# Kernel optimization log

Measured on AMD Instinct MI355X. Metric: run time of the kernel, lower is better.

The kernel has to match this reference:

```python
import jax, jax.numpy as jnp
import numpy as np

B, C, H, W = 2, 64, 128, 128
KH = KW = 3
K = KH * KW
PAD = 1
GROUPS = 8          # conv groups
OFF_GROUPS = 8      # offset groups (offset channels = 2*OFF_GROUPS*K = 144)
NEG_SLOPE = 0.1


def setup_inputs() -> dict:
    key = jax.random.key(0)
    ks = jax.random.split(key, 8)
    s = lambda fan: 1.0 / np.sqrt(fan)
    return {
        "previous_features": jax.random.normal(ks[0], (B, C, H, W), jnp.float32),
        "offsets": jax.random.normal(ks[1], (B, 2 * OFF_GROUPS * K, H, W), jnp.float32),
        "dcn_weight": jax.random.normal(ks[2], (C, C // GROUPS, KH, KW), jnp.float32) * s((C // GROUPS) * K),
        "dcn_bias": jax.random.normal(ks[3], (C,), jnp.float32) * 0.01,
        "w1": jax.random.normal(ks[4], (C, 2 * C, KH, KW), jnp.float32) * s(2 * C * K),
        "b1": jax.random.normal(ks[5], (C,), jnp.float32) * 0.01,
        "w2": jax.random.normal(ks[6], (C, C, KH, KW), jnp.float32) * s(C * K),
        "b2": jax.random.normal(ks[7], (C,), jnp.float32) * 0.01,
    }


def _deform_conv2d(x, offsets, weight, bias):
    """torchvision DeformConv2d, stride=1, pad=1, dil=1, 3x3.
    x: [B,C,H,W]; offsets: [B, 2*og*K, H, W] with per-tap (dy, dx) pairs.
    """
    b, c, h, w = x.shape
    og = offsets.shape[1] // (2 * K)
    cg_off = c // og
    # [B, og, K, 2, H, W] -> dy, dx each [B, og, K, H, W]
    off = offsets.reshape(b, og, K, 2, h, w)
    dy, dx = off[:, :, :, 0], off[:, :, :, 1]
    # base sampling grid per kernel tap
    by = jnp.repeat(jnp.arange(KH), KW).astype(x.dtype)   # [K]
    bx = jnp.tile(jnp.arange(KW), KH).astype(x.dtype)     # [K]
    py = jnp.arange(h, dtype=x.dtype)[None, None, None, :, None] - PAD \
         + by[None, None, :, None, None] + dy              # [B,og,K,H,W]
    px = jnp.arange(w, dtype=x.dtype)[None, None, None, None, :] - PAD \
         + bx[None, None, :, None, None] + dx

    y0 = jnp.floor(py); x0 = jnp.floor(px)
    wy = py - y0;       wx = px - x0
    y0i = y0.astype(jnp.int32); x0i = x0.astype(jnp.int32)

    xg = x.reshape(b, og, cg_off, h * w)  # channel-grouped, flat spatial

    def samp(yi, xi):
        valid = (yi >= 0) & (yi < h) & (xi >= 0) & (xi < w)
        idx = jnp.clip(yi, 0, h - 1) * w + jnp.clip(xi, 0, w - 1)   # [B,og,K,H,W]
        v = jnp.take_along_axis(xg, idx.reshape(b, og, 1, K * h * w), axis=-1)
        v = v.reshape(b, og, cg_off, K, h, w)
        return v * valid[:, :, None].astype(x.dtype)

    v00 = samp(y0i,     x0i)
    v01 = samp(y0i,     x0i + 1)
    v10 = samp(y0i + 1, x0i)
    v11 = samp(y0i + 1, x0i + 1)
    wy_ = wy[:, :, None]; wx_ = wx[:, :, None]  # [B,og,1,K,H,W]
    sampled = (v00 * (1 - wy_) * (1 - wx_) + v01 * (1 - wy_) * wx_
               + v10 * wy_ * (1 - wx_) + v11 * wy_ * wx_)   # [B,og,Cg,K,H,W]

    g = c // weight.shape[1]
    cg = c // g
    cols = sampled.reshape(b, g, cg, K, h, w)                # channel order preserved
    w_g = weight.reshape(g, cg, cg, K)                       # [g, cout/g, cin/g, K]
    out = jnp.einsum('goik,bgikhw->bgohw', w_g, cols).reshape(b, c, h, w)
    return out + bias[None, :, None, None]


def _conv3x3(x, w, b):
    out = jax.lax.conv_general_dilated(
        x, w, window_strides=(1, 1), padding='SAME',
        dimension_numbers=('NCHW', 'OIHW', 'NCHW'))
    return out + b[None, :, None, None]


def _lrelu(x):
    return jnp.where(x >= 0, x, NEG_SLOPE * x)


def reference(previous_features, offsets, dcn_weight, dcn_bias, w1, b1, w2, b2):
    aligned = _deform_conv2d(previous_features, offsets, dcn_weight, dcn_bias)
    r = jnp.concatenate([aligned, previous_features], axis=1)
    r = _lrelu(_conv3x3(r, w1, b1))
    r = _lrelu(_conv3x3(r, w2, b2))
    return aligned + r
```

## Files before the change

kernel.cpp:

```cpp
#include <hip/hip_runtime.h>
#include <stdint.h>

typedef short short8 __attribute__((ext_vector_type(8)));
typedef float f32x4 __attribute__((ext_vector_type(4)));
typedef unsigned int u32x4 __attribute__((ext_vector_type(4)));
typedef unsigned int u32x2 __attribute__((ext_vector_type(2)));

constexpr int B_ = 2, C_ = 64, H_ = 128, W_ = 128, HW_ = H_ * W_;
constexpr float NEG_SLOPE = 0.1f;

__device__ inline unsigned short f2bf(float f) {
    union { float f; unsigned u; } c; c.f = f;
    unsigned r = c.u + 0x7FFFu + ((c.u >> 16) & 1u);
    return (unsigned short)(r >> 16);
}
__device__ inline float bf2f(unsigned short s) {
    union { unsigned u; float f; } c; c.u = ((unsigned)s) << 16; return c.f;
}
__device__ inline float bflo(unsigned u) {
    union { unsigned u; float f; } c; c.u = u << 16; return c.f;
}
__device__ inline float bfhi(unsigned u) {
    union { unsigned u; float f; } c; c.u = u & 0xFFFF0000u; return c.f;
}

__global__ __launch_bounds__(256) void prep_pack(
    const float* __restrict__ x,  const float* __restrict__ w1,
    const float* __restrict__ w2, const float* __restrict__ dw,
    unsigned short* __restrict__ x_g, unsigned short* __restrict__ w1a,
    unsigned short* __restrict__ w2a, unsigned short* __restrict__ dwr)
{
    __shared__ unsigned short t[64][72];
    const int bx = blockIdx.x;
    const int tid = threadIdx.x;

    if (bx < 512) {
        const int b  = bx >> 8;
        const int p0 = (bx & 255) * 64;
#pragma unroll
        for (int u = tid; u < 4096; u += 256) {
            const int c = u >> 6, pp = u & 63;
            t[pp][c ^ ((pp & 7) << 3)] = f2bf(x[((size_t)b * 64 + c) * HW_ + p0 + pp]);
        }
        __syncthreads();
#pragma unroll
        for (int u = tid; u < 512; u += 256) {
            const int g = u >> 6, pp = u & 63;
            const u32x4 v = *(const u32x4*)&t[pp][(g ^ (pp & 7)) * 8];
            *(u32x4*)(x_g + (((size_t)b * 8 + g) * HW_ + p0 + pp) * 8) = v;
        }
        return;
    }

    const int idx = (bx - 512) * 256 + tid;
    if (idx < 64 * 1152) {
        const int ici = idx & 31, t2 = idx >> 5;
        const int oc = t2 & 63, ks = t2 >> 6;
        const int icc = ks / 9, tap = ks - icc * 9;
        w1a[idx] = f2bf(w1[(oc * 128 + icc * 32 + ici) * 9 + tap]);
    }
    if (idx < 64 * 576) {
        const int ici = idx & 31, t2 = idx >> 5;
        const int oc = t2 & 63, ks = t2 >> 6;
        const int icc = ks / 9, tap = ks - icc * 9;
        w2a[idx] = f2bf(w2[(oc * 64 + icc * 32 + ici) * 9 + tap]);
    }
    if (idx < 8 * 3 * 64 * 8) {
        const int g = idx / 1536, r = idx - g * 1536;
        const int c = r / 512, r2 = r - c * 512;
        const int lane = r2 >> 3, j = r2 & 7;
        const int hi = lane >> 4, l15 = lane & 15;
        const int tp = c * 4 + hi;
        float v = 0.f;
        if (l15 < 8 && tp < 9) v = dw[((g * 8 + l15) * 8 + j) * 9 + tp];
        dwr[idx] = f2bf(v);
    }
}

__global__ __launch_bounds__(256) void dcn_mfma(
    const unsigned short* __restrict__ x_g,
    const float* __restrict__ off,
    const unsigned short* __restrict__ dwr,
    const float* __restrict__ bias,
    unsigned short* __restrict__ al_cl)
{
    const int tid  = threadIdx.x;
    const int wv   = tid >> 6;
    const int lane = tid & 63;
    const int hi   = lane >> 4;
    const int l15  = lane & 15;
    const int tile = blockIdx.x;
    const int b    = tile >> 10;
    const int p    = ((tile & 1023) << 4) + l15;
    const int h    = p >> 7;
    const int w    = p & (W_ - 1);

#pragma unroll
    for (int gi = 0; gi < 2; ++gi) {
        const int g = wv + gi * 4;
        const unsigned short* xg = x_g + ((size_t)b * 8 + g) * HW_ * 8;
        const float* offp = off + ((size_t)b * 144 + g * 18) * HW_ + p;

        float dy0 = offp[(hi * 2 + 0) * HW_];
        float dx0 = offp[(hi * 2 + 1) * HW_];
        float dy1 = offp[((4 + hi) * 2 + 0) * HW_];
        float dx1 = offp[((4 + hi) * 2 + 1) * HW_];
        float dy2 = 0.f, dx2 = 0.f;
        if (hi == 0) { dy2 = offp[16 * HW_]; dx2 = offp[17 * HW_]; }

        u32x4 cr[3][4];
        float fw[3][4];
#pragma unroll
        for (int s = 0; s < 3; ++s) {
            const bool active = (s < 2) || (hi == 0);
            if (active) {
                const int t = s * 4 + hi;
                const float dy = (s == 0) ? dy0 : (s == 1) ? dy1 : dy2;
                const float dx = (s == 0) ? dx0 : (s == 1) ? dx1 : dx2;
                const float py = (float)(h - 1 + t / 3) + dy;
                const float px = (float)(w - 1 + t % 3) + dx;
                const float y0f = floorf(py), x0f = floorf(px);
                const int y0 = (int)y0f, x0 = (int)x0f;
                const int y1 = y0 + 1,  x1 = x0 + 1;
                const float wy = py - y0f, wx = px - x0f;

                const bool vy0 = (unsigned)y0 < (unsigned)H_;
                const bool vy1 = (unsigned)y1 < (unsigned)H_;
                const bool vx0 = (unsigned)x0 < (unsigned)W_;
                const bool vx1 = (unsigned)x1 < (unsigned)W_;

                fw[s][0] = (vy0 && vx0) ? (1.f - wy) * (1.f - wx) : 0.f;
                fw[s][1] = (vy0 && vx1) ? (1.f - wy) * wx         : 0.f;
                fw[s][2] = (vy1 && vx0) ? wy * (1.f - wx)         : 0.f;
                fw[s][3] = (vy1 && vx1) ? wy * wx                 : 0.f;

                const int cy0 = min(max(y0, 0), H_ - 1);
                const int cy1 = min(max(y1, 0), H_ - 1);
                const int cx0 = min(max(x0, 0), W_ - 1);
                const int cx1 = min(max(x1, 0), W_ - 1);

                cr[s][0] = *(const u32x4*)(xg + (size_t)(cy0 * W_ + cx0) * 8);
                cr[s][1] = *(const u32x4*)(xg + (size_t)(cy0 * W_ + cx1) * 8);
                cr[s][2] = *(const u32x4*)(xg + (size_t)(cy1 * W_ + cx0) * 8);
                cr[s][3] = *(const u32x4*)(xg + (size_t)(cy1 * W_ + cx1) * 8);
            }
        }

        f32x4 acc = (f32x4){0.f, 0.f, 0.f, 0.f};
#pragma unroll
        for (int s = 0; s < 3; ++s) {
            short8 bfr = (short8){0, 0, 0, 0, 0, 0, 0, 0};
            if ((s < 2) || (hi == 0)) {
                unsigned rq[4];
#pragma unroll
                for (int q = 0; q < 4; ++q) {
                    const float lo = fw[s][0] * bflo(cr[s][0][q]) + fw[s][1] * bflo(cr[s][1][q])
                                   + fw[s][2] * bflo(cr[s][2][q]) + fw[s][3] * bflo(cr[s][3][q]);
                    const float hi_ = fw[s][0] * bfhi(cr[s][0][q]) + fw[s][1] * bfhi(cr[s][1][q])
                                    + fw[s][2] * bfhi(cr[s][2][q]) + fw[s][3] * bfhi(cr[s][3][q]);
                    asm("v_cvt_pk_bf16_f32 %0, %1, %2" : "=v"(rq[q]) : "v"(lo), "v"(hi_));
                }
                bfr = *(const short8*)rq;
            }
            const short8 afr = *(const short8*)(dwr + ((g * 3 + s) * 64 + lane) * 8);
            acc = __builtin_amdgcn_mfma_f32_16x16x32_bf16(afr, bfr, acc, 0, 0, 0);
        }

        if (hi < 2) {
            unsigned short o4[4];
#pragma unroll
            for (int r = 0; r < 4; ++r)
                o4[r] = f2bf(acc[r] + bias[g * 8 + hi * 4 + r]);
            *(u32x2*)(al_cl + ((size_t)b * HW_ + p) * 64 + g * 8 + hi * 4) = *(u32x2*)o4;
        }
    }
}

template <int CIN, bool FINAL>
__global__ __launch_bounds__(256) void conv_mfma(
    const unsigned short* __restrict__ in0,
    const unsigned short* __restrict__ x_g,
    const unsigned short* __restrict__ wa,
    const float* __restrict__ bias,
    const unsigned short* __restrict__ resid_cl,
    float* __restrict__ outf,
    unsigned short* __restrict__ outb)
{
    constexpr int NICC = CIN / 32;
    __shared__ unsigned short b_lds[2][3 * 66 * 32];

    const int tid  = threadIdx.x;
    const int lane = tid & 63;
    const int l15  = lane & 15;
    const int hi   = lane >> 4;
    const int wp   = (tid >> 6) & 1;
    const int wo   = tid >> 7;
    const int ct   = blockIdx.x;
    const int row  = blockIdx.y;
    const int b    = blockIdx.z;
    const int col0 = ct * 64;
    const int oc0w = wo * 32;

    f32x4 acc[2][2];
#pragma unroll
    for (int fm = 0; fm < 2; ++fm)
#pragma unroll
        for (int fn = 0; fn < 2; ++fn)
            acc[fm][fn] = (f32x4){0.f, 0.f, 0.f, 0.f};

    u32x4 sreg[4];

    auto ldregs = [&](int icc) {
#pragma unroll
        for (int t = 0; t < 4; ++t) {
            const int u = tid + t * 256;
            u32x4 v = (u32x4){0u, 0u, 0u, 0u};
            if (u < 792) {
                const int icq = u & 3, rc = u >> 2;
                const int ri = rc / 66, hc = rc - ri * 66;
                const int gr = row + ri - 1, gc = col0 + hc - 1;
                if ((unsigned)gr < 128u && (unsigned)gc < 128u) {
                    const int pix = gr * 128 + gc;
                    if (CIN == 64 || icc < 2)
                        v = *(const u32x4*)(in0 + ((size_t)b * HW_ + pix) * 64
                                             + icc * 32 + icq * 8);
                    else {
                        const int g = (icc - 2) * 4 + icq;
                        v = *(const u32x4*)(x_g + (((size_t)b * 8 + g) * HW_ + pix) * 8);
                    }
                }
            }
            sreg[t] = v;
        }
    };

    auto dswrite = [&](int buf) {
        char* bp = (char*)b_lds[buf];
#pragma unroll
        for (int t = 0; t < 4; ++t) {
            const int u = tid + t * 256;
            if (u < 792) {
                const int icq = u & 3, rc = u >> 2;
                const int hc = rc % 66;
                *(u32x4*)(bp + ((rc * 64 + icq * 16) ^ ((hc & 7) << 4))) = sreg[t];
            }
        }
    };

    auto compute = [&](int icc, int buf) {
        const char* bp = (const char*)b_lds[buf];
#pragma unroll
        for (int tap = 0; tap < 9; ++tap) {
            const int tr = tap / 3, tc = tap - tr * 3;
            short8 af[2], bfr[2];
#pragma unroll
            for (int fm = 0; fm < 2; ++fm)
                af[fm] = *(const short8*)(wa +
                    ((size_t)((icc * 9 + tap) * 64) + oc0w + fm * 16 + l15) * 32 + hi * 8);
#pragma unroll
            for (int fn = 0; fn < 2; ++fn) {
                const int hcol = wp * 32 + fn * 16 + l15 + tc;
                bfr[fn] = *(const short8*)(bp +
                    (((tr * 66 + hcol) * 64 + hi * 16) ^ ((hcol & 7) << 4)));
            }
#pragma unroll
            for (int fm = 0; fm < 2; ++fm)
#pragma unroll
                for (int fn = 0; fn < 2; ++fn)
                    acc[fm][fn] = __builtin_amdgcn_mfma_f32_16x16x32_bf16(
                        af[fm], bfr[fn], acc[fm][fn], 0, 0, 0);
        }
    };

    ldregs(0);
    dswrite(0);
    __syncthreads();
#pragma unroll
    for (int icc = 0; icc < NICC; ++icc) {
        if (icc + 1 < NICC) ldregs(icc + 1);
        compute(icc, icc & 1);
        if (icc + 1 < NICC) {
            dswrite((icc + 1) & 1);
            __syncthreads();
        }
    }

    const int prow = row * 128 + col0 + wp * 32;
    if (!FINAL) {
#pragma unroll
        for (int fm = 0; fm < 2; ++fm)
#pragma unroll
            for (int fn = 0; fn < 2; ++fn) {
                const int px = prow + fn * 16 + l15;
                unsigned short o4[4];
#pragma unroll
                for (int r = 0; r < 4; ++r) {
                    const int oc = oc0w + fm * 16 + hi * 4 + r;
                    float v = acc[fm][fn][r] + bias[oc];
                    v = (v >= 0.f) ? v : NEG_SLOPE * v;
                    o4[r] = f2bf(v);
                }
                *(u32x2*)(outb + ((size_t)b * HW_ + px) * 64 + oc0w + fm * 16 + hi * 4)
                    = *(u32x2*)o4;
            }
    } else {
#pragma unroll
        for (int fm = 0; fm < 2; ++fm)
#pragma unroll
            for (int fn = 0; fn < 2; ++fn) {
                const int px = prow + fn * 16 + l15;
                const size_t gp = (size_t)b * HW_ + px;
                u32x2 alv = *(const u32x2*)(resid_cl + gp * 64 + oc0w + fm * 16 + hi * 4);
                unsigned short alu[4];
                *(u32x2*)alu = alv;
#pragma unroll
                for (int r = 0; r < 4; ++r) {
                    const int oc = oc0w + fm * 16 + hi * 4 + r;
                    float v = acc[fm][fn][r] + bias[oc];
                    v = (v >= 0.f) ? v : NEG_SLOPE * v;
                    v += bf2f(alu[r]);
                    outf[((size_t)b * C_ + oc) * HW_ + px] = v;
                }
            }
    }
}

extern "C" void kernel_launch(void* const* d_in, const int* in_sizes, int n_in,
                              void* d_out, int out_size, void* d_ws, size_t ws_size,
                              hipStream_t stream) {
    const float* x   = (const float*)d_in[0];
    const float* off = (const float*)d_in[1];
    const float* dw  = (const float*)d_in[2];
    const float* db  = (const float*)d_in[3];
    const float* w1  = (const float*)d_in[4];
    const float* b1  = (const float*)d_in[5];
    const float* w2  = (const float*)d_in[6];
    const float* b2  = (const float*)d_in[7];
    float* out = (float*)d_out;

    unsigned short* al_cl = (unsigned short*)d_ws;
    unsigned short* x_g   = al_cl + (size_t)B_ * HW_ * 64;
    unsigned short* t1_cl = x_g + (size_t)B_ * HW_ * 64;
    unsigned short* w1a   = t1_cl + (size_t)B_ * HW_ * 64;
    unsigned short* w2a   = w1a + 64 * 1152;
    unsigned short* dwr   = w2a + 64 * 576;

    prep_pack<<<512 + 288, 256, 0, stream>>>(x, w1, w2, dw, x_g, w1a, w2a, dwr);
    dcn_mfma<<<B_ * HW_ / 16, 256, 0, stream>>>(x_g, off, dwr, db, al_cl);
    conv_mfma<128, false><<<dim3(2, H_, B_), 256, 0, stream>>>(
        al_cl, x_g, w1a, b1, nullptr, nullptr, t1_cl);
    conv_mfma<64, true><<<dim3(2, H_, B_), 256, 0, stream>>>(
        t1_cl, nullptr, w2a, b2, al_cl, out, nullptr);
}
```

Before: 56.46 us.

## Switch intermediates to fp16 with packed-half bilinear math and split DCN grid

Switches every packed intermediate (x, weights, aligned, t1) from bf16 to fp16 and uses f16 MFMA throughout. The bilinear interpolation in the deformable conv now runs as packed half2 FMAs instead of per-element fp32 unpack and multiply with a bf16 repack, cutting ALU work. The DCN kernel also launches twice as many blocks, each handling four offset groups instead of looping over eight, which adds parallelism and lowers register pressure. The risks are fp16 range limits and the precision of the bilinear weights rounded to half.

```diff
diff --git a/kernel.cpp b/kernel.cpp
--- a/kernel.cpp
+++ b/kernel.cpp
@@ -1,7 +1,8 @@
 #include <hip/hip_runtime.h>
 #include <stdint.h>
 
-typedef short short8 __attribute__((ext_vector_type(8)));
+typedef _Float16 h2 __attribute__((ext_vector_type(2)));
+typedef _Float16 half8 __attribute__((ext_vector_type(8)));
 typedef float f32x4 __attribute__((ext_vector_type(4)));
 typedef unsigned int u32x4 __attribute__((ext_vector_type(4)));
 typedef unsigned int u32x2 __attribute__((ext_vector_type(2)));
@@ -9,19 +10,18 @@
 constexpr int B_ = 2, C_ = 64, H_ = 128, W_ = 128, HW_ = H_ * W_;
 constexpr float NEG_SLOPE = 0.1f;
 
-__device__ inline unsigned short f2bf(float f) {
-    union { float f; unsigned u; } c; c.f = f;
-    unsigned r = c.u + 0x7FFFu + ((c.u >> 16) & 1u);
-    return (unsigned short)(r >> 16);
-}
-__device__ inline float bf2f(unsigned short s) {
-    union { unsigned u; float f; } c; c.u = ((unsigned)s) << 16; return c.f;
-}
-__device__ inline float bflo(unsigned u) {
-    union { unsigned u; float f; } c; c.u = u << 16; return c.f;
-}
-__device__ inline float bfhi(unsigned u) {
-    union { unsigned u; float f; } c; c.u = u & 0xFFFF0000u; return c.f;
+__device__ inline unsigned short f2h(float f) {
+    _Float16 h = (_Float16)f;
+    union { _Float16 h; unsigned short s; } c; c.h = h; return c.s;
+}
+__device__ inline float h2f(unsigned short s) {
+    union { unsigned short s; _Float16 h; } c; c.s = s; return (float)c.h;
+}
+__device__ inline h2 u2h2(unsigned u) {
+    union { unsigned u; h2 h; } c; c.u = u; return c.h;
+}
+__device__ inline unsigned h22u(h2 h) {
+    union { unsigned u; h2 h; } c; c.h = h; return c.u;
 }
 
 __global__ __launch_bounds__(256) void prep_pack(
@@ -40,7 +40,7 @@
 #pragma unroll
         for (int u = tid; u < 4096; u += 256) {
             const int c = u >> 6, pp = u & 63;
-            t[pp][c ^ ((pp & 7) << 3)] = f2bf(x[((size_t)b * 64 + c) * HW_ + p0 + pp]);
+            t[pp][c ^ ((pp & 7) << 3)] = f2h(x[((size_t)b * 64 + c) * HW_ + p0 + pp]);
         }
         __syncthreads();
 #pragma unroll
@@ -57,13 +57,13 @@
         const int ici = idx & 31, t2 = idx >> 5;
         const int oc = t2 & 63, ks = t2 >> 6;
         const int icc = ks / 9, tap = ks - icc * 9;
-        w1a[idx] = f2bf(w1[(oc * 128 + icc * 32 + ici) * 9 + tap]);
+        w1a[idx] = f2h(w1[(oc * 128 + icc * 32 + ici) * 9 + tap]);
     }
     if (idx < 64 * 576) {
         const int ici = idx & 31, t2 = idx >> 5;
         const int oc = t2 & 63, ks = t2 >> 6;
         const int icc = ks / 9, tap = ks - icc * 9;
-        w2a[idx] = f2bf(w2[(oc * 64 + icc * 32 + ici) * 9 + tap]);
+        w2a[idx] = f2h(w2[(oc * 64 + icc * 32 + ici) * 9 + tap]);
     }
     if (idx < 8 * 3 * 64 * 8) {
         const int g = idx / 1536, r = idx - g * 1536;
@@ -73,7 +73,7 @@
         const int tp = c * 4 + hi;
         float v = 0.f;
         if (l15 < 8 && tp < 9) v = dw[((g * 8 + l15) * 8 + j) * 9 + tp];
-        dwr[idx] = f2bf(v);
+        dwr[idx] = f2h(v);
     }
 }
 
@@ -89,90 +89,93 @@
     const int lane = tid & 63;
     const int hi   = lane >> 4;
     const int l15  = lane & 15;
-    const int tile = blockIdx.x;
+    const int bx   = blockIdx.x;
+    const int tile = bx & 2047;
+    const int gq   = bx >> 11;
     const int b    = tile >> 10;
     const int p    = ((tile & 1023) << 4) + l15;
     const int h    = p >> 7;
     const int w    = p & (W_ - 1);
 
-#pragma unroll
-    for (int gi = 0; gi < 2; ++gi) {
-        const int g = wv + gi * 4;
-        const unsigned short* xg = x_g + ((size_t)b * 8 + g) * HW_ * 8;
-        const float* offp = off + ((size_t)b * 144 + g * 18) * HW_ + p;
-
-        float dy0 = offp[(hi * 2 + 0) * HW_];
-        float dx0 = offp[(hi * 2 + 1) * HW_];
-        float dy1 = offp[((4 + hi) * 2 + 0) * HW_];
-        float dx1 = offp[((4 + hi) * 2 + 1) * HW_];
-        float dy2 = 0.f, dx2 = 0.f;
-        if (hi == 0) { dy2 = offp[16 * HW_]; dx2 = offp[17 * HW_]; }
-
-        u32x4 cr[3][4];
-        float fw[3][4];
-#pragma unroll
-        for (int s = 0; s < 3; ++s) {
-            const bool active = (s < 2) || (hi == 0);
-            if (active) {
-                const int t = s * 4 + hi;
-                const float dy = (s == 0) ? dy0 : (s == 1) ? dy1 : dy2;
-                const float dx = (s == 0) ? dx0 : (s == 1) ? dx1 : dx2;
-                const float py = (float)(h - 1 + t / 3) + dy;
-                const float px = (float)(w - 1 + t % 3) + dx;
-                const float y0f = floorf(py), x0f = floorf(px);
-                const int y0 = (int)y0f, x0 = (int)x0f;
-                const int y1 = y0 + 1,  x1 = x0 + 1;
-                const float wy = py - y0f, wx = px - x0f;
-
-                const bool vy0 = (unsigned)y0 < (unsigned)H_;
-                const bool vy1 = (unsigned)y1 < (unsigned)H_;
-                const bool vx0 = (unsigned)x0 < (unsigned)W_;
-                const bool vx1 = (unsigned)x1 < (unsigned)W_;
-
-                fw[s][0] = (vy0 && vx0) ? (1.f - wy) * (1.f - wx) : 0.f;
-                fw[s][1] = (vy0 && vx1) ? (1.f - wy) * wx         : 0.f;
-                fw[s][2] = (vy1 && vx0) ? wy * (1.f - wx)         : 0.f;
-                fw[s][3] = (vy1 && vx1) ? wy * wx                 : 0.f;
-
-                const int cy0 = min(max(y0, 0), H_ - 1);
-                const int cy1 = min(max(y1, 0), H_ - 1);
-                const int cx0 = min(max(x0, 0), W_ - 1);
-                const int cx1 = min(max(x1, 0), W_ - 1);
-
-                cr[s][0] = *(const u32x4*)(xg + (size_t)(cy0 * W_ + cx0) * 8);
-                cr[s][1] = *(const u32x4*)(xg + (size_t)(cy0 * W_ + cx1) * 8);
-                cr[s][2] = *(const u32x4*)(xg + (size_t)(cy1 * W_ + cx0) * 8);
-                cr[s][3] = *(const u32x4*)(xg + (size_t)(cy1 * W_ + cx1) * 8);
-            }
-        }
-
-        f32x4 acc = (f32x4){0.f, 0.f, 0.f, 0.f};
-#pragma unroll
-        for (int s = 0; s < 3; ++s) {
-            short8 bfr = (short8){0, 0, 0, 0, 0, 0, 0, 0};
-            if ((s < 2) || (hi == 0)) {
-                unsigned rq[4];
-#pragma unroll
-                for (int q = 0; q < 4; ++q) {
-                    const float lo = fw[s][0] * bflo(cr[s][0][q]) + fw[s][1] * bflo(cr[s][1][q])
-                                   + fw[s][2] * bflo(cr[s][2][q]) + fw[s][3] * bflo(cr[s][3][q]);
-                    const float hi_ = fw[s][0] * bfhi(cr[s][0][q]) + fw[s][1] * bfhi(cr[s][1][q])
-                                    + fw[s][2] * bfhi(cr[s][2][q]) + fw[s][3] * bfhi(cr[s][3][q]);
-                    asm("v_cvt_pk_bf16_f32 %0, %1, %2" : "=v"(rq[q]) : "v"(lo), "v"(hi_));
-                }
-                bfr = *(const short8*)rq;
-            }
-            const short8 afr = *(const short8*)(dwr + ((g * 3 + s) * 64 + lane) * 8);
-            acc = __builtin_amdgcn_mfma_f32_16x16x32_bf16(afr, bfr, acc, 0, 0, 0);
-        }
-
-        if (hi < 2) {
-            unsigned short o4[4];
-#pragma unroll
-            for (int r = 0; r < 4; ++r)
-                o4[r] = f2bf(acc[r] + bias[g * 8 + hi * 4 + r]);
-            *(u32x2*)(al_cl + ((size_t)b * HW_ + p) * 64 + g * 8 + hi * 4) = *(u32x2*)o4;
-        }
+    const int g = wv + gq * 4;
+    const unsigned short* xg = x_g + ((size_t)b * 8 + g) * HW_ * 8;
+    const float* offp = off + ((size_t)b * 144 + g * 18) * HW_ + p;
+
+    float dy0 = offp[(hi * 2 + 0) * HW_];
+    float dx0 = offp[(hi * 2 + 1) * HW_];
+    float dy1 = offp[((4 + hi) * 2 + 0) * HW_];
+    float dx1 = offp[((4 + hi) * 2 + 1) * HW_];
+    float dy2 = 0.f, dx2 = 0.f;
+    if (hi == 0) { dy2 = offp[16 * HW_]; dx2 = offp[17 * HW_]; }
+
+    u32x4 cr[3][4];
+    float fw[3][4];
+#pragma unroll
+    for (int s = 0; s < 3; ++s) {
+        const bool active = (s < 2) || (hi == 0);
+        if (active) {
+            const int t = s * 4 + hi;
+            const float dy = (s == 0) ? dy0 : (s == 1) ? dy1 : dy2;
+            const float dx = (s == 0) ? dx0 : (s == 1) ? dx1 : dx2;
+            const float py = (float)(h - 1 + t / 3) + dy;
+            const float px = (float)(w - 1 + t % 3) + dx;
+            const float y0f = floorf(py), x0f = floorf(px);
+            const int y0 = (int)y0f, x0 = (int)x0f;
+            const int y1 = y0 + 1,  x1 = x0 + 1;
+            const float wy = py - y0f, wx = px - x0f;
+
+            const bool vy0 = (unsigned)y0 < (unsigned)H_;
+            const bool vy1 = (unsigned)y1 < (unsigned)H_;
+            const bool vx0 = (unsigned)x0 < (unsigned)W_;
+            const bool vx1 = (unsigned)x1 < (unsigned)W_;
+
+            fw[s][0] = (vy0 && vx0) ? (1.f - wy) * (1.f - wx) : 0.f;
+            fw[s][1] = (vy0 && vx1) ? (1.f - wy) * wx         : 0.f;
+            fw[s][2] = (vy1 && vx0) ? wy * (1.f - wx)         : 0.f;
+            fw[s][3] = (vy1 && vx1) ? wy * wx                 : 0.f;
+
+            const int cy0 = min(max(y0, 0), H_ - 1);
+            const int cy1 = min(max(y1, 0), H_ - 1);
+            const int cx0 = min(max(x0, 0), W_ - 1);
+            const int cx1 = min(max(x1, 0), W_ - 1);
+
+            cr[s][0] = *(const u32x4*)(xg + (size_t)(cy0 * W_ + cx0) * 8);
+            cr[s][1] = *(const u32x4*)(xg + (size_t)(cy0 * W_ + cx1) * 8);
+            cr[s][2] = *(const u32x4*)(xg + (size_t)(cy1 * W_ + cx0) * 8);
+            cr[s][3] = *(const u32x4*)(xg + (size_t)(cy1 * W_ + cx1) * 8);
+        }
+    }
+
+    f32x4 acc = (f32x4){0.f, 0.f, 0.f, 0.f};
+#pragma unroll
+    for (int s = 0; s < 3; ++s) {
+        half8 bfr = (half8){0, 0, 0, 0, 0, 0, 0, 0};
+        if ((s < 2) || (hi == 0)) {
+            const h2 f0 = (h2){(_Float16)fw[s][0], (_Float16)fw[s][0]};
+            const h2 f1 = (h2){(_Float16)fw[s][1], (_Float16)fw[s][1]};
+            const h2 f2 = (h2){(_Float16)fw[s][2], (_Float16)fw[s][2]};
+            const h2 f3 = (h2){(_Float16)fw[s][3], (_Float16)fw[s][3]};
+            unsigned rq[4];
+#pragma unroll
+            for (int q = 0; q < 4; ++q) {
+                h2 r = u2h2(cr[s][0][q]) * f0;
+                r = u2h2(cr[s][1][q]) * f1 + r;
+                r = u2h2(cr[s][2][q]) * f2 + r;
+                r = u2h2(cr[s][3][q]) * f3 + r;
+                rq[q] = h22u(r);
+            }
+            bfr = *(const half8*)rq;
+        }
+        const half8 afr = *(const half8*)(dwr + ((g * 3 + s) * 64 + lane) * 8);
+        acc = __builtin_amdgcn_mfma_f32_16x16x32_f16(afr, bfr, acc, 0, 0, 0);
+    }
+
+    if (hi < 2) {
+        unsigned short o4[4];
+#pragma unroll
+        for (int r = 0; r < 4; ++r)
+            o4[r] = f2h(acc[r] + bias[g * 8 + hi * 4 + r]);
+        *(u32x2*)(al_cl + ((size_t)b * HW_ + p) * 64 + g * 8 + hi * 4) = *(u32x2*)o4;
     }
 }
 
@@ -252,22 +255,22 @@
 #pragma unroll
         for (int tap = 0; tap < 9; ++tap) {
             const int tr = tap / 3, tc = tap - tr * 3;
-            short8 af[2], bfr[2];
+            half8 af[2], bfr[2];
 #pragma unroll
             for (int fm = 0; fm < 2; ++fm)
-                af[fm] = *(const short8*)(wa +
+                af[fm] = *(const half8*)(wa +
                     ((size_t)((icc * 9 + tap) * 64) + oc0w + fm * 16 + l15) * 32 + hi * 8);
 #pragma unroll
             for (int fn = 0; fn < 2; ++fn) {
                 const int hcol = wp * 32 + fn * 16 + l15 + tc;
-                bfr[fn] = *(const short8*)(bp +
+                bfr[fn] = *(const half8*)(bp +
                     (((tr * 66 + hcol) * 64 + hi * 16) ^ ((hcol & 7) << 4)));
             }
 #pragma unroll
             for (int fm = 0; fm < 2; ++fm)
 #pragma unroll
                 for (int fn = 0; fn < 2; ++fn)
-                    acc[fm][fn] = __builtin_amdgcn_mfma_f32_16x16x32_bf16(
+                    acc[fm][fn] = __builtin_amdgcn_mfma_f32_16x16x32_f16(
                         af[fm], bfr[fn], acc[fm][fn], 0, 0, 0);
         }
     };
@@ -298,7 +301,7 @@
                     const int oc = oc0w + fm * 16 + hi * 4 + r;
                     float v = acc[fm][fn][r] + bias[oc];
                     v = (v >= 0.f) ? v : NEG_SLOPE * v;
-                    o4[r] = f2bf(v);
+                    o4[r] = f2h(v);
                 }
                 *(u32x2*)(outb + ((size_t)b * HW_ + px) * 64 + oc0w + fm * 16 + hi * 4)
                     = *(u32x2*)o4;
@@ -318,7 +321,7 @@
                     const int oc = oc0w + fm * 16 + hi * 4 + r;
                     float v = acc[fm][fn][r] + bias[oc];
                     v = (v >= 0.f) ? v : NEG_SLOPE * v;
-                    v += bf2f(alu[r]);
+                    v += h2f(alu[r]);
                     outf[((size_t)b * C_ + oc) * HW_ + px] = v;
                 }
             }
@@ -346,7 +349,7 @@
     unsigned short* dwr   = w2a + 64 * 576;
 
     prep_pack<<<512 + 288, 256, 0, stream>>>(x, w1, w2, dw, x_g, w1a, w2a, dwr);
-    dcn_mfma<<<B_ * HW_ / 16, 256, 0, stream>>>(x_g, off, dwr, db, al_cl);
+    dcn_mfma<<<2 * B_ * HW_ / 16, 256, 0, stream>>>(x_g, off, dwr, db, al_cl);
     conv_mfma<128, false><<<dim3(2, H_, B_), 256, 0, stream>>>(
         al_cl, x_g, w1a, b1, nullptr, nullptr, t1_cl);
     conv_mfma<64, true><<<dim3(2, H_, B_), 256, 0, stream>>>(
```

Result: faster. 55.29 us (-2.1%).
